# Kernel optimization log

Measured on AMD Instinct MI355X. Metric: run time of the kernel, lower is better.

The kernel has to match this reference:

```python
import jax, jax.numpy as jnp
import numpy as np

FILTERS = [1, 3, 7, 9]
BN_EPS = 1e-5


def _conv1d(x, w, b):
    # x: [B, C, L], w: [O, I, F] (torch Conv1d layout), 'same' padding for odd F
    pad = (w.shape[-1] - 1) // 2
    y = jax.lax.conv_general_dilated(
        x, w, window_strides=(1,), padding=[(pad, pad)],
        dimension_numbers=("NCH", "OIH", "NCH"))
    return y + b[None, :, None]


def _bn_elu(x, gamma, beta):
    # BatchNorm1d in training mode: biased batch stats over (batch, length)
    m = jnp.mean(x, axis=(0, 2), keepdims=True)
    v = jnp.var(x, axis=(0, 2), keepdims=True)
    xn = (x - m) * jax.lax.rsqrt(v + BN_EPS)
    return jax.nn.elu(xn * gamma[None, :, None] + beta[None, :, None])


def setup_inputs() -> dict:
    key = jax.random.key(0)
    ks = jax.random.split(key, 32)
    b, h, l, lk, dk = 8, 8, 1024, 1024, 64
    inp = {
        "Q": jax.random.normal(ks[0], (b, h, l, dk), jnp.float32),
        "K": jax.random.normal(ks[1], (b, h, lk, dk), jnp.float32),
        "V": jax.random.normal(ks[2], (b, h, lk, dk), jnp.float32),
        "W_pq": jax.random.normal(ks[3], (1, dk), jnp.float32) * 0.1,
        "W_bq": jax.random.normal(ks[4], (dk, 1), jnp.float32) * 0.1,
        "W_bk": jax.random.normal(ks[5], (dk, 1), jnp.float32) * 0.1,
        "bn_g": jax.random.uniform(ks[6], (h,), jnp.float32, 0.5, 1.5),
        "bn_b": jax.random.normal(ks[7], (h,), jnp.float32) * 0.1,
        "attn_mask": jnp.ones((1,), dtype=bool),
    }
    for i, f in enumerate(FILTERS):
        s = 1.0 / np.sqrt(h * f)
        inp[f"cq_w{i}"] = jax.random.normal(ks[8 + i], (h, h, f), jnp.float32) * s
        inp[f"cq_b{i}"] = jax.random.normal(ks[12 + i], (h,), jnp.float32) * 0.05
        inp[f"ck_w{i}"] = jax.random.normal(ks[16 + i], (h, h, f), jnp.float32) * s
        inp[f"ck_b{i}"] = jax.random.normal(ks[20 + i], (h,), jnp.float32) * 0.05
    return inp


def reference(Q, K, V, W_pq, W_bq, W_bk,
              cq_w0, cq_b0, cq_w1, cq_b1, cq_w2, cq_b2, cq_w3, cq_b3,
              ck_w0, ck_b0, ck_w1, ck_b1, ck_w2, ck_b2, ck_w3, ck_b3,
              bn_g, bn_b, attn_mask):
    b, h, l, dk = Q.shape
    lk = K.shape[2]
    nf = len(FILTERS)
    # proj_q applied to BOTH Q and K (proj_k is dead in the original code)
    q = jnp.einsum("bhld,d->bhl", Q, W_pq[0])  # [b,h,l]
    k = jnp.einsum("bhld,d->bhl", K, W_pq[0])  # [b,h,lk]
    cq = [(cq_w0, cq_b0), (cq_w1, cq_b1), (cq_w2, cq_b2), (cq_w3, cq_b3)]
    ck = [(ck_w0, ck_b0), (ck_w1, ck_b1), (ck_w2, ck_b2), (ck_w3, ck_b3)]
    Q_l = [_bn_elu(_conv1d(q, w, bb), bn_g, bn_b) for w, bb in cq]
    K_l = [_bn_elu(_conv1d(k, w, bb), bn_g, bn_b) for w, bb in ck]
    # replicate torch.cat(dim=0) + reshape(b,h,nf*len) flat-order semantics
    Q_p = jnp.concatenate(Q_l, axis=0).reshape(b, h, nf * l)    # [b,h,4l]
    K_p = jnp.concatenate(K_l, axis=0).reshape(b, h, nf * lk)   # [b,h,4lk]
    Qt = jax.lax.top_k(Q_p, l)[0]                               # [b,h,l]
    Km = jnp.mean(K_p.reshape(b, h, nf, lk), axis=2)            # [b,h,lk]
    Kt = jax.lax.top_k(Km, lk)[0]                               # descending sort
    Qb = Qt[..., None] * W_bq[:, 0]                             # [b,h,l,dk]
    Kb = Kt[..., None] * W_bk[:, 0]                             # [b,h,lk,dk]
    scores = jnp.einsum("bhqd,bhkd->bhqk", Qb, Kb) / np.float32(np.sqrt(dk))
    attn = jax.nn.softmax(scores, axis=-1)
    context = jnp.einsum("bhqk,bhkd->bhqd", attn, V)
    return context, attn
```

## Files before the change

kernel.cpp:

```cpp
#include <hip/hip_runtime.h>
#include <hip/hip_bf16.h>
#include <math.h>

namespace {
constexpr int PROJ_OFF = 0;
constexpr int CONV_OFF = 131072;
constexpr int PS_OFF   = 655360;
constexpr int PSS_OFF  = 657408;
constexpr int QT_OFF   = 659456;
constexpr int KT_OFF   = 724992;

typedef short bf16x8 __attribute__((ext_vector_type(8)));
typedef float f32x4 __attribute__((ext_vector_type(4)));

union BF8 {
  bf16x8 v;
  short s[8];
};

__device__ inline void lgkm_barrier() {
  __builtin_amdgcn_sched_barrier(0);
  asm volatile("s_waitcnt lgkmcnt(0)" ::: "memory");
  __builtin_amdgcn_s_barrier();
  __builtin_amdgcn_sched_barrier(0);
}

__global__ __launch_bounds__(256) void proj_kernel(
    const float* __restrict__ Q, const float* __restrict__ K,
    const float* __restrict__ Wpq, float* __restrict__ proj) {
  __shared__ float wsh[64];
  const int tid = threadIdx.x;
  if (tid < 64) wsh[tid] = Wpq[tid];
  __syncthreads();
  const int row = blockIdx.x * 256 + tid;
  const float* src = (row < 65536) ? (Q + (size_t)row * 64)
                                   : (K + (size_t)(row - 65536) * 64);
  float acc = 0.f;
#pragma unroll
  for (int j = 0; j < 16; ++j) {
    const float4 v = *(const float4*)(src + j * 4);
    acc = fmaf(v.x, wsh[j * 4 + 0], acc);
    acc = fmaf(v.y, wsh[j * 4 + 1], acc);
    acc = fmaf(v.z, wsh[j * 4 + 2], acc);
    acc = fmaf(v.w, wsh[j * 4 + 3], acc);
  }
  proj[row] = acc;
}

template <int F>
__device__ void conv_body(const float* __restrict__ xs,
                          const float* __restrict__ wsm,
                          const float* __restrict__ bsm,
                          float* __restrict__ outp, int tid, int lq,
                          float accs[8]) {
  constexpr int pad = (F - 1) / 2;
#pragma unroll
  for (int j = 0; j < 8; ++j) {
    float acc = bsm[j];
#pragma unroll
    for (int c = 0; c < 8; ++c) {
      const float* xrow = &xs[c * 264 + tid + 4 - pad];
      const float* wrow = &wsm[(j * 8 + c) * F];
#pragma unroll
      for (int f = 0; f < F; ++f) acc = fmaf(xrow[f], wrow[f], acc);
    }
    outp[j * 1024 + lq * 256 + tid] = acc;
    accs[j] = acc;
  }
}

__global__ __launch_bounds__(256) void conv_kernel(
    const float* __restrict__ proj,
    const float* __restrict__ wq0, const float* __restrict__ bq0,
    const float* __restrict__ wq1, const float* __restrict__ bq1,
    const float* __restrict__ wq2, const float* __restrict__ bq2,
    const float* __restrict__ wq3, const float* __restrict__ bq3,
    const float* __restrict__ wk0, const float* __restrict__ bk0,
    const float* __restrict__ wk1, const float* __restrict__ bk1,
    const float* __restrict__ wk2, const float* __restrict__ bk2,
    const float* __restrict__ wk3, const float* __restrict__ bk3,
    float* __restrict__ conv, float* __restrict__ psum,
    float* __restrict__ psumsq) {
  __shared__ float xs[8 * 264];
  __shared__ float wsm[8 * 8 * 9];
  __shared__ float bsm[8];
  __shared__ float redS[8][4], redSS[8][4];
  const int tid = threadIdx.x;
  const int blk = blockIdx.x;
  const int path = blk >> 7, fi = (blk >> 5) & 3, bb = (blk >> 2) & 7;
  const int lq = blk & 3;
  const int F = (0x9731 >> (fi * 4)) & 0xF;
  const float* wp;
  const float* bp;
  if (path == 0) {
    wp = fi == 0 ? wq0 : fi == 1 ? wq1 : fi == 2 ? wq2 : wq3;
    bp = fi == 0 ? bq0 : fi == 1 ? bq1 : fi == 2 ? bq2 : bq3;
  } else {
    wp = fi == 0 ? wk0 : fi == 1 ? wk1 : fi == 2 ? wk2 : wk3;
    bp = fi == 0 ? bk0 : fi == 1 ? bk1 : fi == 2 ? bk2 : bk3;
  }
  const float* pb = proj + path * 65536 + bb * 8192;
  for (int e = tid; e < 8 * 264; e += 256) {
    const int c = e / 264, pos = e - c * 264;
    const int gl = lq * 256 + pos - 4;
    xs[e] = (gl >= 0 && gl < 1024) ? pb[c * 1024 + gl] : 0.f;
  }
  for (int e = tid; e < 64 * F; e += 256) wsm[e] = wp[e];
  if (tid < 8) bsm[tid] = bp[tid];
  __syncthreads();
  float* outp = conv + ((size_t)(path * 4 + fi) * 8 + bb) * 8192;
  float accs[8];
  if (fi == 0)
    conv_body<1>(xs, wsm, bsm, outp, tid, lq, accs);
  else if (fi == 1)
    conv_body<3>(xs, wsm, bsm, outp, tid, lq, accs);
  else if (fi == 2)
    conv_body<7>(xs, wsm, bsm, outp, tid, lq, accs);
  else
    conv_body<9>(xs, wsm, bsm, outp, tid, lq, accs);
  const int lane = tid & 63, wv = tid >> 6;
#pragma unroll
  for (int j = 0; j < 8; ++j) {
    float sv = accs[j], qv = accs[j] * accs[j];
#pragma unroll
    for (int mm = 32; mm >= 1; mm >>= 1) {
      sv += __shfl_xor(sv, mm, 64);
      qv += __shfl_xor(qv, mm, 64);
    }
    if (lane == 0) {
      redS[j][wv] = sv;
      redSS[j][wv] = qv;
    }
  }
  __syncthreads();
  if (tid < 16) {
    const int j = tid & 7;
    const bool wantss = tid >= 8;
    const float* rr = wantss ? &redSS[j][0] : &redS[j][0];
    const float tot = rr[0] + rr[1] + rr[2] + rr[3];
    float* dst = wantss ? psumsq : psum;
    dst[((path * 4 + fi) * 8 + j) * 32 + bb * 4 + lq] = tot;
  }
}

__device__ inline float bn_elu(float v, float mean, float rstd, float g,
                               float be) {
  const float x = (v - mean) * rstd * g + be;
  return x > 0.f ? x : expm1f(x);
}

__device__ inline void cswap(float& a, float& b, bool up) {
  const float mx = fmaxf(a, b), mn = fminf(a, b);
  a = up ? mx : mn;
  b = up ? mn : mx;
}

__device__ inline void shfl_pass(float v[4], int t, int m, bool up) {
  const bool keepmax = (up == ((t & m) == 0));
#pragma unroll
  for (int e = 0; e < 4; ++e) {
    const float p = __shfl_xor(v[e], m, 64);
    v[e] = keepmax ? fmaxf(v[e], p) : fminf(v[e], p);
  }
}

__device__ inline void lds_pass(float v[4], float* s, int t, int jq, bool up) {
  *(float4*)&s[4 * t] = make_float4(v[0], v[1], v[2], v[3]);
  __syncthreads();
  const int pt = t ^ jq;
  const bool keepmax = (up == ((t & jq) == 0));
  const float4 p = *(const float4*)&s[4 * pt];
  v[0] = keepmax ? fmaxf(v[0], p.x) : fminf(v[0], p.x);
  v[1] = keepmax ? fmaxf(v[1], p.y) : fminf(v[1], p.y);
  v[2] = keepmax ? fmaxf(v[2], p.z) : fminf(v[2], p.z);
  v[3] = keepmax ? fmaxf(v[3], p.w) : fminf(v[3], p.w);
  __syncthreads();
}

__device__ inline void reg_tail(float v[4], int t, bool up) {
#pragma unroll
  for (int m = 32; m >= 1; m >>= 1) shfl_pass(v, t, m, up);
  cswap(v[0], v[2], up);
  cswap(v[1], v[3], up);
  cswap(v[0], v[1], up);
  cswap(v[2], v[3], up);
}

__device__ inline void sort1024(float v[4], float* s, int t) {
  cswap(v[0], v[1], true);
  cswap(v[2], v[3], false);
#pragma unroll
  for (int k = 4; k <= 256; k <<= 1) {
    const bool up = ((t & (k >> 2)) == 0);
    for (int m = k >> 3; m >= 1; m >>= 1) shfl_pass(v, t, m, up);
    cswap(v[0], v[2], up);
    cswap(v[1], v[3], up);
    cswap(v[0], v[1], up);
    cswap(v[2], v[3], up);
  }
  {
    const bool up = ((t & 128) == 0);
    lds_pass(v, s, t, 64, up);
    reg_tail(v, t, up);
  }
  lds_pass(v, s, t, 128, true);
  lds_pass(v, s, t, 64, true);
  reg_tail(v, t, true);
}

__device__ inline void bmerge1024(float v[4], float* s, int t) {
  lds_pass(v, s, t, 128, true);
  lds_pass(v, s, t, 64, true);
  reg_tail(v, t, true);
}

__global__ __launch_bounds__(256) void sortmerge_kernel(
    const float* __restrict__ conv, const float* __restrict__ psum,
    const float* __restrict__ psumsq, const float* __restrict__ bng,
    const float* __restrict__ bnb, float* __restrict__ Qt,
    float* __restrict__ Kt) {
  __shared__ float s[1024];
  __shared__ float sred[8];
  __shared__ float cm[4], cr[4];
  const int t = threadIdx.x, blk = blockIdx.x;
  const bool isQ = blk < 64;
  const int row = isQ ? blk : blk - 64;
  const int hp = row & 7;
  const int fi = row >> 4;
  const int bb = ((row >> 3) & 1) * 4 + (hp >> 1);
  const int chbase = (isQ ? 0 : 32) + fi * 8 + (hp & 1) * 4;
  if (t < 8) {
    const float* src = (t < 4) ? psum : psumsq;
    const int ch = chbase + (t & 3);
    float a = 0.f;
    for (int i = 0; i < 32; ++i) a += src[ch * 32 + i];
    sred[t] = a;
  }
  __syncthreads();
  if (t < 4) {
    const float mean = sred[t] * (1.f / 8192.f);
    const float var = sred[4 + t] * (1.f / 8192.f) - mean * mean;
    cm[t] = mean;
    cr[t] = rsqrtf(fmaxf(var, 0.f) + 1e-5f);
  }
  __syncthreads();
  if (isQ) {
    const float* base = conv + (size_t)(fi * 8 + bb) * 8192;
    float c0[4], c1[4], c2[4], c3[4];
#pragma unroll
    for (int jc = 0; jc < 4; ++jc) {
      float* v = jc == 0 ? c0 : jc == 1 ? c1 : jc == 2 ? c2 : c3;
      const int hh = (hp & 1) * 4 + jc;
      const float mean = cm[jc], rstd = cr[jc];
      const float g = bng[hh], be = bnb[hh];
      const float4 x = *(const float4*)&base[hh * 1024 + 4 * t];
      v[0] = bn_elu(x.x, mean, rstd, g, be);
      v[1] = bn_elu(x.y, mean, rstd, g, be);
      v[2] = bn_elu(x.z, mean, rstd, g, be);
      v[3] = bn_elu(x.w, mean, rstd, g, be);
      sort1024(v, s, t);
    }
    float a[4], b[4];
    *(float4*)&s[4 * t] = make_float4(c1[0], c1[1], c1[2], c1[3]);
    __syncthreads();
#pragma unroll
    for (int e = 0; e < 4; ++e) a[e] = fmaxf(c0[e], s[1023 - 4 * t - e]);
    __syncthreads();
    bmerge1024(a, s, t);
    *(float4*)&s[4 * t] = make_float4(c3[0], c3[1], c3[2], c3[3]);
    __syncthreads();
#pragma unroll
    for (int e = 0; e < 4; ++e) b[e] = fmaxf(c2[e], s[1023 - 4 * t - e]);
    __syncthreads();
    bmerge1024(b, s, t);
    *(float4*)&s[4 * t] = make_float4(b[0], b[1], b[2], b[3]);
    __syncthreads();
#pragma unroll
    for (int e = 0; e < 4; ++e) a[e] = fmaxf(a[e], s[1023 - 4 * t - e]);
    __syncthreads();
    bmerge1024(a, s, t);
    *(float4*)&Qt[(size_t)row * 1024 + 4 * t] =
        make_float4(a[0], a[1], a[2], a[3]);
  } else {
    float v[4];
    float sum0 = 0.f, sum1 = 0.f, sum2 = 0.f, sum3 = 0.f;
#pragma unroll
    for (int j = 0; j < 4; ++j) {
      const int hh = (hp & 1) * 4 + j;
      const float mean = cm[j], rstd = cr[j];
      const float g = bng[hh], be = bnb[hh];
      const float4 x = *(const float4*)&conv[(size_t)(4 + fi) * 64 * 1024 +
                                             (size_t)bb * 8192 + hh * 1024 +
                                             4 * t];
      sum0 += bn_elu(x.x, mean, rstd, g, be);
      sum1 += bn_elu(x.y, mean, rstd, g, be);
      sum2 += bn_elu(x.z, mean, rstd, g, be);
      sum3 += bn_elu(x.w, mean, rstd, g, be);
    }
    v[0] = sum0 * 0.25f;
    v[1] = sum1 * 0.25f;
    v[2] = sum2 * 0.25f;
    v[3] = sum3 * 0.25f;
    sort1024(v, s, t);
    *(float4*)&Kt[(size_t)row * 1024 + 4 * t] =
        make_float4(v[0], v[1], v[2], v[3]);
  }
}

__global__ __launch_bounds__(256, 4) void attn7_kernel(
    const float* __restrict__ V, const float* __restrict__ Qt,
    const float* __restrict__ Kt, const float* __restrict__ Wbq,
    const float* __restrict__ Wbk, float* __restrict__ ctx,
    float* __restrict__ attn) {
  __shared__ float Kts[1024];
  __shared__ float sq[64], cz[64], msh[64];
  __shared__ short Vhi[2][8 * 64 * 8];
  __shared__ short Vlo[2][8 * 64 * 8];
  const int tid = threadIdx.x;
  const int b = blockIdx.x;
  const int bh = ((b & 7) << 3) | ((b >> 3) & 7);
  const int qt = b >> 6;
  const int qbase = qt * 64;
  const int lane0 = tid & 63;
  float cval;
  {
    float d = Wbq[lane0] * Wbk[lane0];
#pragma unroll
    for (int mm = 32; mm >= 1; mm >>= 1) d += __shfl_xor(d, mm, 64);
    cval = d * 0.125f;
  }
  const float* Ktg = Kt + (size_t)bh * 1024;
  for (int t = tid; t < 1024; t += 256) Kts[t] = Ktg[t];
  const float kHi = Ktg[0], kLo = Ktg[1023];
  if (tid < 64) {
    const float s = cval * Qt[(size_t)bh * 1024 + qbase + tid];
    sq[tid] = s;
    msh[tid] = fmaxf(s * kHi, s * kLo);
  }
  __syncthreads();
  {
    const int row = tid >> 2, qtr = tid & 3;
    const float s = sq[row], m = msh[row];
    float z = 0.f;
    const int k0 = qtr * 256;
    for (int k = 0; k < 256; ++k) z += __expf(fmaf(s, Kts[k0 + k], -m));
    z += __shfl_xor(z, 1, 64);
    z += __shfl_xor(z, 2, 64);
    if (qtr == 0) cz[row] = -m - __logf(z);
  }
  __syncthreads();

  const int wv = tid >> 6, l = tid & 63;
  const int l15 = l & 15, l4 = l >> 4;
  const int q = wv * 16 + l15;
  const float s = sq[q], c = cz[q];
  f32x4 acc[4];
#pragma unroll
  for (int dt = 0; dt < 4; ++dt) acc[dt] = (f32x4){0.f, 0.f, 0.f, 0.f};

  const float* Vb = V + (size_t)bh * 65536;
  float* arow = attn + ((size_t)bh << 20) + (size_t)qbase * 1024;
  const int dV = tid & 63, kqV = tid >> 6;

  float vreg[2][8];
#pragma unroll
  for (int g = 0; g < 2; ++g) {
    const float* vs = Vb + (size_t)((kqV + g * 4) * 8) * 64 + dV;
#pragma unroll
    for (int i = 0; i < 8; ++i) vreg[g][i] = vs[i * 64];
  }

  for (int ch = 0; ch < 16; ++ch) {
    const int kc = ch * 64;
    const int buf = ch & 1;
    bf16x8 ahi[2], alo[2];
    float4 est[2][2];
#pragma unroll
    for (int ks = 0; ks < 2; ++ks) {
      const int kb = kc + ks * 32 + l4 * 8;
      const float4 kv0 = *(const float4*)&Kts[kb];
      const float4 kv1 = *(const float4*)&Kts[kb + 4];
      float e[8];
      e[0] = __expf(fmaf(s, kv0.x, c));
      e[1] = __expf(fmaf(s, kv0.y, c));
      e[2] = __expf(fmaf(s, kv0.z, c));
      e[3] = __expf(fmaf(s, kv0.w, c));
      e[4] = __expf(fmaf(s, kv1.x, c));
      e[5] = __expf(fmaf(s, kv1.y, c));
      e[6] = __expf(fmaf(s, kv1.z, c));
      e[7] = __expf(fmaf(s, kv1.w, c));
      est[ks][0] = make_float4(e[0], e[1], e[2], e[3]);
      est[ks][1] = make_float4(e[4], e[5], e[6], e[7]);
      BF8 H, L;
#pragma unroll
      for (int i = 0; i < 8; ++i) {
        const __hip_bfloat16 hb = __float2bfloat16(e[i]);
        H.s[i] = __bfloat16_as_short(hb);
        L.s[i] =
            __bfloat16_as_short(__float2bfloat16(e[i] - __bfloat162float(hb)));
      }
      ahi[ks] = H.v;
      alo[ks] = L.v;
    }
#pragma unroll
    for (int g = 0; g < 2; ++g) {
      const int ko = kqV + g * 4;
      BF8 H, L;
#pragma unroll
      for (int i = 0; i < 8; ++i) {
        const float f = vreg[g][i];
        const __hip_bfloat16 hb = __float2bfloat16(f);
        H.s[i] = __bfloat16_as_short(hb);
        L.s[i] =
            __bfloat16_as_short(__float2bfloat16(f - __bfloat162float(hb)));
      }
      *(bf16x8*)&Vhi[buf][(ko * 64 + dV) * 8] = H.v;
      *(bf16x8*)&Vlo[buf][(ko * 64 + dV) * 8] = L.v;
    }
    lgkm_barrier();
    if (ch < 15) {
#pragma unroll
      for (int g = 0; g < 2; ++g) {
        const float* vs =
            Vb + (size_t)(kc + 64 + (kqV + g * 4) * 8) * 64 + dV;
#pragma unroll
        for (int i = 0; i < 8; ++i) vreg[g][i] = vs[i * 64];
      }
    }
#pragma unroll
    for (int ks = 0; ks < 2; ++ks) {
      float* ag = arow + (size_t)q * 1024 + kc + ks * 32 + l4 * 8;
      *(float4*)ag = est[ks][0];
      *(float4*)(ag + 4) = est[ks][1];
    }
#pragma unroll
    for (int ks = 0; ks < 2; ++ks) {
      const int ko = ks * 4 + l4;
#pragma unroll
      for (int dt = 0; dt < 4; ++dt) {
        const bf16x8 bhv =
            *(const bf16x8*)&Vhi[buf][(ko * 64 + dt * 16 + l15) * 8];
        const bf16x8 blv =
            *(const bf16x8*)&Vlo[buf][(ko * 64 + dt * 16 + l15) * 8];
        acc[dt] = __builtin_amdgcn_mfma_f32_16x16x32_bf16(ahi[ks], bhv,
                                                          acc[dt], 0, 0, 0);
        acc[dt] = __builtin_amdgcn_mfma_f32_16x16x32_bf16(ahi[ks], blv,
                                                          acc[dt], 0, 0, 0);
        acc[dt] = __builtin_amdgcn_mfma_f32_16x16x32_bf16(alo[ks], bhv,
                                                          acc[dt], 0, 0, 0);
      }
    }
  }
  float* cb = ctx + ((size_t)bh * 1024 + qbase + wv * 16 + l4 * 4) * 64 + l15;
#pragma unroll
  for (int dt = 0; dt < 4; ++dt)
#pragma unroll
    for (int rr = 0; rr < 4; ++rr) cb[(size_t)rr * 64 + dt * 16] = acc[dt][rr];
}

}

extern "C" void kernel_launch(void* const* d_in, const int* in_sizes, int n_in,
                              void* d_out, int out_size, void* d_ws,
                              size_t ws_size, hipStream_t stream) {
  const float* Q = (const float*)d_in[0];
  const float* K = (const float*)d_in[1];
  const float* V = (const float*)d_in[2];
  const float* Wpq = (const float*)d_in[3];
  const float* Wbq = (const float*)d_in[4];
  const float* Wbk = (const float*)d_in[5];
  const float* bng = (const float*)d_in[6];
  const float* bnb = (const float*)d_in[7];
  const float* cqw[4] = {(const float*)d_in[9], (const float*)d_in[13],
                         (const float*)d_in[17], (const float*)d_in[21]};
  const float* cqb[4] = {(const float*)d_in[10], (const float*)d_in[14],
                         (const float*)d_in[18], (const float*)d_in[22]};
  const float* ckw[4] = {(const float*)d_in[11], (const float*)d_in[15],
                         (const float*)d_in[19], (const float*)d_in[23]};
  const float* ckb[4] = {(const float*)d_in[12], (const float*)d_in[16],
                         (const float*)d_in[20], (const float*)d_in[24]};

  float* ws = (float*)d_ws;
  float* proj = ws + PROJ_OFF;
  float* conv = ws + CONV_OFF;
  float* psum = ws + PS_OFF;
  float* psumsq = ws + PSS_OFF;
  float* Qtp = ws + QT_OFF;
  float* Ktp = ws + KT_OFF;
  float* ctx = (float*)d_out;
  float* attn = ctx + (size_t)8 * 8 * 1024 * 64;

  proj_kernel<<<512, 256, 0, stream>>>(Q, K, Wpq, proj);
  conv_kernel<<<256, 256, 0, stream>>>(
      proj, cqw[0], cqb[0], cqw[1], cqb[1], cqw[2], cqb[2], cqw[3], cqb[3],
      ckw[0], ckb[0], ckw[1], ckb[1], ckw[2], ckb[2], ckw[3], ckb[3], conv,
      psum, psumsq);
  sortmerge_kernel<<<128, 256, 0, stream>>>(conv, psum, psumsq, bng, bnb, Qtp,
                                            Ktp);
  attn7_kernel<<<1024, 256, 0, stream>>>(V, Qtp, Ktp, Wbq, Wbk, ctx, attn);
}
```

Before: 122.4 us.

## Split attention into separate softmax-write and context kernels

Splits the fused attention kernel into two. The first writes the normalized attention matrix plus per-row scale and log-normalizer to workspace, using a one-pass row softmax. The second reads those values and computes the context with bf16-split MFMA, no longer storing attn. This takes the large attn store stream off the MFMA kernel so stores and matrix math no longer contend, at the cost of an extra launch and recomputing exponentials in both kernels. The new sq/cz buffers reuse the proj workspace region, which is dead by then.

```diff
diff --git a/kernel.cpp b/kernel.cpp
--- a/kernel.cpp
+++ b/kernel.cpp
@@ -9,6 +9,8 @@
 constexpr int PSS_OFF  = 657408;
 constexpr int QT_OFF   = 659456;
 constexpr int KT_OFF   = 724992;
+constexpr int SQ_OFF   = 0;
+constexpr int CZ_OFF   = 65536;
 
 typedef short bf16x8 __attribute__((ext_vector_type(8)));
 typedef float f32x4 __attribute__((ext_vector_type(4)));
@@ -307,13 +309,69 @@
   }
 }
 
-__global__ __launch_bounds__(256, 4) void attn7_kernel(
-    const float* __restrict__ V, const float* __restrict__ Qt,
-    const float* __restrict__ Kt, const float* __restrict__ Wbq,
-    const float* __restrict__ Wbk, float* __restrict__ ctx,
-    float* __restrict__ attn) {
+__global__ __launch_bounds__(256) void attnw_kernel(
+    const float* __restrict__ Qt, const float* __restrict__ Kt,
+    const float* __restrict__ Wbq, const float* __restrict__ Wbk,
+    float* __restrict__ attn, float* __restrict__ sqw,
+    float* __restrict__ czw) {
   __shared__ float Kts[1024];
-  __shared__ float sq[64], cz[64], msh[64];
+  const int tid = threadIdx.x;
+  const int b = blockIdx.x;
+  const int bh = ((b & 7) << 3) | ((b >> 3) & 7);
+  const int qt = b >> 6;
+  const int qbase = qt * 32;
+  const int wv = tid >> 6, l = tid & 63;
+  float cval;
+  {
+    float d = Wbq[l] * Wbk[l];
+#pragma unroll
+    for (int mm = 32; mm >= 1; mm >>= 1) d += __shfl_xor(d, mm, 64);
+    cval = d * 0.125f;
+  }
+  const float* Ktg = Kt + (size_t)bh * 1024;
+  for (int t = tid; t < 1024; t += 256) Kts[t] = Ktg[t];
+  const float kHi = Ktg[0], kLo = Ktg[1023];
+  __syncthreads();
+  float* arow = attn + ((size_t)bh << 20) + (size_t)qbase * 1024;
+  const float* Qrow = Qt + (size_t)bh * 1024 + qbase;
+#pragma unroll 2
+  for (int r = 0; r < 8; ++r) {
+    const int q = wv * 8 + r;
+    const float s = cval * Qrow[q];
+    const float m = fmaxf(s * kHi, s * kLo);
+    float e[16];
+    float z = 0.f;
+#pragma unroll
+    for (int j = 0; j < 4; ++j) {
+      const float4 kv = *(const float4*)&Kts[j * 256 + l * 4];
+      e[j * 4 + 0] = __expf(fmaf(s, kv.x, -m));
+      e[j * 4 + 1] = __expf(fmaf(s, kv.y, -m));
+      e[j * 4 + 2] = __expf(fmaf(s, kv.z, -m));
+      e[j * 4 + 3] = __expf(fmaf(s, kv.w, -m));
+      z += (e[j * 4 + 0] + e[j * 4 + 1]) + (e[j * 4 + 2] + e[j * 4 + 3]);
+    }
+#pragma unroll
+    for (int mm = 32; mm >= 1; mm >>= 1) z += __shfl_xor(z, mm, 64);
+    const float rz = 1.f / z;
+    if (l == 0) {
+      sqw[(size_t)bh * 1024 + qbase + q] = s;
+      czw[(size_t)bh * 1024 + qbase + q] = -m - __logf(z);
+    }
+    float* ag = arow + (size_t)q * 1024;
+#pragma unroll
+    for (int j = 0; j < 4; ++j)
+      *(float4*)&ag[j * 256 + l * 4] =
+          make_float4(e[j * 4 + 0] * rz, e[j * 4 + 1] * rz, e[j * 4 + 2] * rz,
+                      e[j * 4 + 3] * rz);
+  }
+}
+
+__global__ __launch_bounds__(256, 4) void attnc_kernel(
+    const float* __restrict__ V, const float* __restrict__ Kt,
+    const float* __restrict__ sqw, const float* __restrict__ czw,
+    float* __restrict__ ctx) {
+  __shared__ float Kts[1024];
+  __shared__ float sq[64], cz[64];
   __shared__ short Vhi[2][8 * 64 * 8];
   __shared__ short Vlo[2][8 * 64 * 8];
   const int tid = threadIdx.x;
@@ -321,32 +379,11 @@
   const int bh = ((b & 7) << 3) | ((b >> 3) & 7);
   const int qt = b >> 6;
   const int qbase = qt * 64;
-  const int lane0 = tid & 63;
-  float cval;
-  {
-    float d = Wbq[lane0] * Wbk[lane0];
-#pragma unroll
-    for (int mm = 32; mm >= 1; mm >>= 1) d += __shfl_xor(d, mm, 64);
-    cval = d * 0.125f;
-  }
   const float* Ktg = Kt + (size_t)bh * 1024;
   for (int t = tid; t < 1024; t += 256) Kts[t] = Ktg[t];
-  const float kHi = Ktg[0], kLo = Ktg[1023];
   if (tid < 64) {
-    const float s = cval * Qt[(size_t)bh * 1024 + qbase + tid];
-    sq[tid] = s;
-    msh[tid] = fmaxf(s * kHi, s * kLo);
-  }
-  __syncthreads();
-  {
-    const int row = tid >> 2, qtr = tid & 3;
-    const float s = sq[row], m = msh[row];
-    float z = 0.f;
-    const int k0 = qtr * 256;
-    for (int k = 0; k < 256; ++k) z += __expf(fmaf(s, Kts[k0 + k], -m));
-    z += __shfl_xor(z, 1, 64);
-    z += __shfl_xor(z, 2, 64);
-    if (qtr == 0) cz[row] = -m - __logf(z);
+    sq[tid] = sqw[(size_t)bh * 1024 + qbase + tid];
+    cz[tid] = czw[(size_t)bh * 1024 + qbase + tid];
   }
   __syncthreads();
 
@@ -359,7 +396,6 @@
   for (int dt = 0; dt < 4; ++dt) acc[dt] = (f32x4){0.f, 0.f, 0.f, 0.f};
 
   const float* Vb = V + (size_t)bh * 65536;
-  float* arow = attn + ((size_t)bh << 20) + (size_t)qbase * 1024;
   const int dV = tid & 63, kqV = tid >> 6;
 
   float vreg[2][8];
@@ -374,7 +410,6 @@
     const int kc = ch * 64;
     const int buf = ch & 1;
     bf16x8 ahi[2], alo[2];
-    float4 est[2][2];
 #pragma unroll
     for (int ks = 0; ks < 2; ++ks) {
       const int kb = kc + ks * 32 + l4 * 8;
@@ -389,8 +424,6 @@
       e[5] = __expf(fmaf(s, kv1.y, c));
       e[6] = __expf(fmaf(s, kv1.z, c));
       e[7] = __expf(fmaf(s, kv1.w, c));
-      est[ks][0] = make_float4(e[0], e[1], e[2], e[3]);
-      est[ks][1] = make_float4(e[4], e[5], e[6], e[7]);
       BF8 H, L;
 #pragma unroll
       for (int i = 0; i < 8; ++i) {
@@ -426,12 +459,6 @@
 #pragma unroll
         for (int i = 0; i < 8; ++i) vreg[g][i] = vs[i * 64];
       }
-    }
-#pragma unroll
-    for (int ks = 0; ks < 2; ++ks) {
-      float* ag = arow + (size_t)q * 1024 + kc + ks * 32 + l4 * 8;
-      *(float4*)ag = est[ks][0];
-      *(float4*)(ag + 4) = est[ks][1];
     }
 #pragma unroll
     for (int ks = 0; ks < 2; ++ks) {
@@ -487,6 +514,8 @@
   float* psumsq = ws + PSS_OFF;
   float* Qtp = ws + QT_OFF;
   float* Ktp = ws + KT_OFF;
+  float* sqw = ws + SQ_OFF;
+  float* czw = ws + CZ_OFF;
   float* ctx = (float*)d_out;
   float* attn = ctx + (size_t)8 * 8 * 1024 * 64;
 
@@ -497,5 +526,6 @@
       psum, psumsq);
   sortmerge_kernel<<<128, 256, 0, stream>>>(conv, psum, psumsq, bng, bnb, Qtp,
                                             Ktp);
-  attn7_kernel<<<1024, 256, 0, stream>>>(V, Qtp, Ktp, Wbq, Wbk, ctx, attn);
-}
+  attnw_kernel<<<2048, 256, 0, stream>>>(Qtp, Ktp, Wbq, Wbk, attn, sqw, czw);
+  attnc_kernel<<<1024, 256, 0, stream>>>(V, Ktp, sqw, czw, ctx);
+}
```

Result: slower. 143.1 us (+16.9%).
